# Kernel optimization log

Measured on AMD Instinct MI355X. Metric: run time of the kernel, lower is better.

The kernel has to match this reference:

```python
import jax, jax.numpy as jnp
import numpy as np

LAGS = 2
SLOPE = 0.2  # leaky_relu negative slope


def setup_inputs() -> dict:
    key = jax.random.key(0)
    ks = jax.random.split(key, 12)
    B, T, D, E, H = 32, 1002, 16, 32, 64  # batch, lags+length, latent, embed, hidden
    s = 0.1
    return {
        "x": jax.random.normal(ks[0], (B, T, D), jnp.float32),
        "embeddings": jax.random.normal(ks[1], (B, T, E), jnp.float32),
        # per-latent-dim stacked MLP2 params (num_layers=3 hidden + output head)
        "W0": jax.random.normal(ks[2], (D, H, E + 1), jnp.float32) * s,
        "b0": jax.random.normal(ks[3], (D, H), jnp.float32) * s,
        "W1": jax.random.normal(ks[4], (D, H, H), jnp.float32) * s,
        "b1": jax.random.normal(ks[5], (D, H), jnp.float32) * s,
        "W2": jax.random.normal(ks[6], (D, H, H), jnp.float32) * s,
        "b2": jax.random.normal(ks[7], (D, H), jnp.float32) * s,
        "Wo": jax.random.normal(ks[8], (D, 1, H), jnp.float32) * s,
        "bo": jax.random.normal(ks[9], (D, 1), jnp.float32) * s,
    }


def reference(x, embeddings, W0, b0, W1, b1, W2, b2, Wo, bo):
    B, TL, D = x.shape
    length = TL - LAGS
    E = embeddings.shape[-1]
    N = B * length

    # last element of each unfolded window == x[:, LAGS:, :]
    x_t = x[:, LAGS:, :].reshape(N, D)                       # [N, D]
    emb = embeddings[:, -length:, :].reshape(N, E)           # [N, E]
    # per-dim input: concat(embedding, x_t[:, i]) -> [N, D, E+1]
    inp = jnp.concatenate(
        [jnp.broadcast_to(emb[:, None, :], (N, D, E)), x_t[:, :, None]], axis=-1
    )

    # batched tiny MLPs across latent dims; keep leaky-relu gates for analytic Jacobian
    z0 = jnp.einsum('dhe,nde->ndh', W0, inp) + b0            # [N, D, H]
    g0 = jnp.where(z0 >= 0, 1.0, SLOPE)
    a0 = z0 * g0
    z1 = jnp.einsum('dij,ndj->ndi', W1, a0) + b1
    g1 = jnp.where(z1 >= 0, 1.0, SLOPE)
    a1 = z1 * g1
    z2 = jnp.einsum('dij,ndj->ndi', W2, a1) + b2
    g2 = jnp.where(z2 >= 0, 1.0, SLOPE)
    a2 = z2 * g2
    res = jnp.einsum('doh,ndh->ndo', Wo, a2)[..., 0] + bo[:, 0]   # [N, D]

    # d residual_i / d x_t_i : propagate last input column through the chain
    t = g0 * W0[:, :, -1]                                    # [N, D, H]
    t = g1 * jnp.einsum('dij,ndj->ndi', W1, t)
    t = g2 * jnp.einsum('dij,ndj->ndi', W2, t)
    dJ = jnp.einsum('doh,ndh->ndo', Wo, t)[..., 0]           # [N, D]

    logabsdet = jnp.sum(jnp.log(jnp.abs(dJ)), axis=-1)       # [N]

    residuals = res.reshape(B, length, D)
    log_abs_det_jacobian = logabsdet.reshape(B, length)
    return residuals, log_abs_det_jacobian
```

## Files before the change

kernel.cpp:

```cpp
#include <hip/hip_runtime.h>

constexpr int   kT    = 1002;
constexpr int   kD    = 16;
constexpr int   kE    = 32;
constexpr int   kH    = 64;
constexpr int   kLen  = kT - 2;
constexpr int   kN    = 32 * kLen;
constexpr float kSlope = 0.2f;
constexpr int   AS    = 68;
constexpr int   kWsDwPerD = 15360;

typedef __attribute__((ext_vector_type(8))) short bf16x8;
typedef __attribute__((ext_vector_type(4))) float f32x4;

__device__ __forceinline__ unsigned rne2(float x0, float x1, float &h0, float &h1) {
    unsigned u0 = __float_as_uint(x0), u1 = __float_as_uint(x1);
    unsigned r0 = u0 + 0x7FFFu + ((u0 >> 16) & 1u);
    unsigned r1 = u1 + 0x7FFFu + ((u1 >> 16) & 1u);
    h0 = __uint_as_float(r0 & 0xFFFF0000u);
    h1 = __uint_as_float(r1 & 0xFFFF0000u);
    return __builtin_amdgcn_perm(r1, r0, 0x07060302u);
}

__device__ __forceinline__ void split3_2(float x0, float x1,
                                         unsigned &p1, unsigned &p2, unsigned &p3) {
    float h0, h1; p1 = rne2(x0, x1, h0, h1);
    float e0 = x0 - h0, e1 = x1 - h1;
    float m0, m1; p2 = rne2(e0, e1, m0, m1);
    float f0 = e0 - m0, f1 = e1 - m1;
    float t0, t1; p3 = rne2(f0, f1, t0, t1);
}

__device__ __forceinline__ void split2_2(float x0, float x1, unsigned &p1, unsigned &p2) {
    float h0, h1; p1 = rne2(x0, x1, h0, h1);
    float t0, t1; p2 = rne2(x0 - h0, x1 - h1, t0, t1);
}

union FragU { unsigned u[4]; bf16x8 v; };

__device__ __forceinline__ void splitA3(const float4 a0, const float4 a1,
                                        bf16x8 &A1, bf16x8 &A2, bf16x8 &A3) {
    FragU U1, U2, U3;
    split3_2(a0.x, a0.y, U1.u[0], U2.u[0], U3.u[0]);
    split3_2(a0.z, a0.w, U1.u[1], U2.u[1], U3.u[1]);
    split3_2(a1.x, a1.y, U1.u[2], U2.u[2], U3.u[2]);
    split3_2(a1.z, a1.w, U1.u[3], U2.u[3], U3.u[3]);
    A1 = U1.v; A2 = U2.v; A3 = U3.v;
}

__device__ __forceinline__ void splitA2(const float4 a0, const float4 a1,
                                        bf16x8 &A1, bf16x8 &A2) {
    FragU U1, U2;
    split2_2(a0.x, a0.y, U1.u[0], U2.u[0]);
    split2_2(a0.z, a0.w, U1.u[1], U2.u[1]);
    split2_2(a1.x, a1.y, U1.u[2], U2.u[2]);
    split2_2(a1.z, a1.w, U1.u[3], U2.u[3]);
    A1 = U1.v; A2 = U2.v;
}

__global__ void prep_weights(const float* __restrict__ W0, const float* __restrict__ W1,
                             const float* __restrict__ W2, unsigned* __restrict__ ws,
                             float* __restrict__ out_ld) {
    int id = blockIdx.x * blockDim.x + threadIdx.x;
    if (id < kN) out_ld[id] = 0.f;
    if (id >= 16 * 5120) return;
    int d = id / 5120, rem = id - d * 5120;
    unsigned* wd = ws + (size_t)d * kWsDwPerD;
    float x0, x1; unsigned o1, o2, o3;
    if (rem < 1024) {
        int idx = rem, j2 = idx & 3, ln = (idx >> 2) & 63, nt = (idx >> 8) & 3;
        int n_ = nt * 16 + (ln & 15), k_ = ((ln >> 4) << 3) + 2 * j2;
        const float* g = W0 + (size_t)d * kH * 33;
        x0 = g[n_ * 33 + k_]; x1 = g[n_ * 33 + k_ + 1];
        o1 = idx; o2 = 1024 + idx; o3 = 2048 + idx;
    } else if (rem < 3072) {
        int idx = rem - 1024, j2 = idx & 3, ln = (idx >> 2) & 63;
        int kt = (idx >> 8) & 1, nt = (idx >> 9) & 3;
        int n_ = nt * 16 + (ln & 15), k_ = kt * 32 + ((ln >> 4) << 3) + 2 * j2;
        const float* g = W1 + (size_t)d * kH * kH;
        x0 = g[n_ * 64 + k_]; x1 = g[n_ * 64 + k_ + 1];
        o1 = 3072 + idx; o2 = 5120 + idx; o3 = 7168 + idx;
    } else {
        int idx = rem - 3072, j2 = idx & 3, ln = (idx >> 2) & 63;
        int kt = (idx >> 8) & 1, nt = (idx >> 9) & 3;
        int n_ = nt * 16 + (ln & 15), k_ = kt * 32 + ((ln >> 4) << 3) + 2 * j2;
        const float* g = W2 + (size_t)d * kH * kH;
        x0 = g[n_ * 64 + k_]; x1 = g[n_ * 64 + k_ + 1];
        o1 = 9216 + idx; o2 = 11264 + idx; o3 = 13312 + idx;
    }
    unsigned p1, p2, p3; split3_2(x0, x1, p1, p2, p3);
    wd[o1] = p1; wd[o2] = p2; wd[o3] = p3;
}

#define MFMA(A, B, C) __builtin_amdgcn_mfma_f32_16x16x32_bf16((A), (B), (C), 0, 0, 0)

__device__ __forceinline__ void layer64_f(f32x4 acc[2][4],
                                          const float* r0, const float* r1,
                                          const unsigned* w1, const unsigned* w2,
                                          const unsigned* w3, int lane, int q) {
    #pragma unroll
    for (int kt = 0; kt < 2; ++kt) {
        bf16x8 A1[2], A2[2], A3[2];
        {
            const float4 a0 = *(const float4*)(r0 + kt * 32 + q * 8);
            const float4 a1 = *(const float4*)(r0 + kt * 32 + q * 8 + 4);
            splitA3(a0, a1, A1[0], A2[0], A3[0]);
            const float4 b0_ = *(const float4*)(r1 + kt * 32 + q * 8);
            const float4 b1_ = *(const float4*)(r1 + kt * 32 + q * 8 + 4);
            splitA3(b0_, b1_, A1[1], A2[1], A3[1]);
        }
        bf16x8 B[4];
        #pragma unroll
        for (int nt = 0; nt < 4; ++nt) B[nt] = *(const bf16x8*)(w1 + (((nt * 2 + kt) * 64 + lane) << 2));
        #pragma unroll
        for (int nt = 0; nt < 4; ++nt)
            #pragma unroll
            for (int mt = 0; mt < 2; ++mt) {
                acc[mt][nt] = MFMA(A3[mt], B[nt], acc[mt][nt]);
                acc[mt][nt] = MFMA(A2[mt], B[nt], acc[mt][nt]);
                acc[mt][nt] = MFMA(A1[mt], B[nt], acc[mt][nt]);
            }
        #pragma unroll
        for (int nt = 0; nt < 4; ++nt) B[nt] = *(const bf16x8*)(w2 + (((nt * 2 + kt) * 64 + lane) << 2));
        #pragma unroll
        for (int nt = 0; nt < 4; ++nt)
            #pragma unroll
            for (int mt = 0; mt < 2; ++mt) {
                acc[mt][nt] = MFMA(A2[mt], B[nt], acc[mt][nt]);
                acc[mt][nt] = MFMA(A1[mt], B[nt], acc[mt][nt]);
            }
        #pragma unroll
        for (int nt = 0; nt < 4; ++nt) B[nt] = *(const bf16x8*)(w3 + (((nt * 2 + kt) * 64 + lane) << 2));
        #pragma unroll
        for (int nt = 0; nt < 4; ++nt)
            #pragma unroll
            for (int mt = 0; mt < 2; ++mt)
                acc[mt][nt] = MFMA(A1[mt], B[nt], acc[mt][nt]);
    }
}

__device__ __forceinline__ void layer64_j(f32x4 acc[2][4],
                                          const float* r0, const float* r1,
                                          const unsigned* w1, const unsigned* w2,
                                          int lane, int q) {
    #pragma unroll
    for (int kt = 0; kt < 2; ++kt) {
        bf16x8 A1[2], A2[2];
        {
            const float4 a0 = *(const float4*)(r0 + kt * 32 + q * 8);
            const float4 a1 = *(const float4*)(r0 + kt * 32 + q * 8 + 4);
            splitA2(a0, a1, A1[0], A2[0]);
            const float4 b0_ = *(const float4*)(r1 + kt * 32 + q * 8);
            const float4 b1_ = *(const float4*)(r1 + kt * 32 + q * 8 + 4);
            splitA2(b0_, b1_, A1[1], A2[1]);
        }
        bf16x8 B[4];
        #pragma unroll
        for (int nt = 0; nt < 4; ++nt) B[nt] = *(const bf16x8*)(w1 + (((nt * 2 + kt) * 64 + lane) << 2));
        #pragma unroll
        for (int nt = 0; nt < 4; ++nt)
            #pragma unroll
            for (int mt = 0; mt < 2; ++mt) {
                acc[mt][nt] = MFMA(A2[mt], B[nt], acc[mt][nt]);
                acc[mt][nt] = MFMA(A1[mt], B[nt], acc[mt][nt]);
            }
        #pragma unroll
        for (int nt = 0; nt < 4; ++nt) B[nt] = *(const bf16x8*)(w2 + (((nt * 2 + kt) * 64 + lane) << 2));
        #pragma unroll
        for (int nt = 0; nt < 4; ++nt)
            #pragma unroll
            for (int mt = 0; mt < 2; ++mt)
                acc[mt][nt] = MFMA(A1[mt], B[nt], acc[mt][nt]);
    }
}

__global__ __launch_bounds__(256, 2) void np_mfma_kernel(
    const float* __restrict__ x, const float* __restrict__ emb,
    const float* __restrict__ W0, const float* __restrict__ b0,
    const float* __restrict__ b1, const float* __restrict__ b2,
    const float* __restrict__ Wo, const float* __restrict__ bo,
    const unsigned* __restrict__ ws,
    float* __restrict__ out_res, float* __restrict__ out_ld)
{
    __shared__ __align__(16) float act[128 * AS];

    const int tid  = threadIdx.x;
    const int lane = tid & 63;
    const int wave = __builtin_amdgcn_readfirstlane(tid >> 6);
    const int c = lane & 15, q = lane >> 4;
    const int tb = wave * 32;
    const int d  = blockIdx.y;
    const int nW = blockIdx.x * 128 + tb;

    {
    }
    const int nX  = nW + ((q >> 1) << 4) + c;
    const int bbX = nX / kLen;
    const float xm = x[((size_t)(bbX * kT + (nX - bbX * kLen) + 2)) * kD + d];
    float xr[2][4];
    #pragma unroll
    for (int mt = 0; mt < 2; ++mt)
        #pragma unroll
        for (int r = 0; r < 4; ++r)
            xr[mt][r] = __shfl(xm, mt * 32 + q * 4 + r, 64);

    const float* W0g = W0 + (size_t)d * kH * 33;
    float b0v[4], wov[4], w0xv[4];
    #pragma unroll
    for (int nt = 0; nt < 4; ++nt) {
        const int u = nt * 16 + c;
        b0v[nt]  = b0[d * kH + u];
        wov[nt]  = Wo[d * kH + u];
        w0xv[nt] = W0g[u * 33 + 32];
    }
    const float bov = bo[d];
    const unsigned* wd = ws + (size_t)d * kWsDwPerD;
    const float* r0 = &act[(tb + c) * AS];
    const float* r1 = &act[(tb + 16 + c) * AS];

    unsigned m0 = 0, m1 = 0, m2 = 0;
    f32x4 acc[2][4];

    {
        bf16x8 A1[2], A2[2], A3[2];
        #pragma unroll
        for (int mt = 0; mt < 2; ++mt) {
            const int nA = nW + mt * 16 + c;
            const int bb = nA / kLen;
            const size_t src = (size_t)(bb * kT + (nA - bb * kLen) + 2);
            const float4* ep = (const float4*)(emb + src * kE + q * 8);
            splitA3(ep[0], ep[1], A1[mt], A2[mt], A3[mt]);
        }
        #pragma unroll
        for (int mt = 0; mt < 2; ++mt)
            #pragma unroll
            for (int nt = 0; nt < 4; ++nt) {
                f32x4 a;
                #pragma unroll
                for (int r = 0; r < 4; ++r) a[r] = fmaf(xr[mt][r], w0xv[nt], b0v[nt]);
                acc[mt][nt] = a;
            }
        bf16x8 B[4];
        #pragma unroll
        for (int nt = 0; nt < 4; ++nt) B[nt] = *(const bf16x8*)(wd + ((nt * 64 + lane) << 2));
        #pragma unroll
        for (int nt = 0; nt < 4; ++nt)
            #pragma unroll
            for (int mt = 0; mt < 2; ++mt) {
                acc[mt][nt] = MFMA(A3[mt], B[nt], acc[mt][nt]);
                acc[mt][nt] = MFMA(A2[mt], B[nt], acc[mt][nt]);
                acc[mt][nt] = MFMA(A1[mt], B[nt], acc[mt][nt]);
            }
        #pragma unroll
        for (int nt = 0; nt < 4; ++nt) B[nt] = *(const bf16x8*)(wd + 1024 + ((nt * 64 + lane) << 2));
        #pragma unroll
        for (int nt = 0; nt < 4; ++nt)
            #pragma unroll
            for (int mt = 0; mt < 2; ++mt) {
                acc[mt][nt] = MFMA(A2[mt], B[nt], acc[mt][nt]);
                acc[mt][nt] = MFMA(A1[mt], B[nt], acc[mt][nt]);
            }
        #pragma unroll
        for (int nt = 0; nt < 4; ++nt) B[nt] = *(const bf16x8*)(wd + 2048 + ((nt * 64 + lane) << 2));
        #pragma unroll
        for (int nt = 0; nt < 4; ++nt)
            #pragma unroll
            for (int mt = 0; mt < 2; ++mt)
                acc[mt][nt] = MFMA(A1[mt], B[nt], acc[mt][nt]);
        #pragma unroll
        for (int mt = 0; mt < 2; ++mt)
            #pragma unroll
            for (int nt = 0; nt < 4; ++nt)
                #pragma unroll
                for (int r = 0; r < 4; ++r) {
                    float z = acc[mt][nt][r];
                    bool g = z >= 0.f;
                    m0 |= (unsigned)g << (mt * 16 + nt * 4 + r);
                    act[(tb + mt * 16 + q * 4 + r) * AS + nt * 16 + c] = g ? z : z * kSlope;
                }
    }

    {
        #pragma unroll
        for (int nt = 0; nt < 4; ++nt) {
            const float bv = b1[d * kH + nt * 16 + c];
            #pragma unroll
            for (int mt = 0; mt < 2; ++mt) {
                f32x4 a;
                #pragma unroll
                for (int r = 0; r < 4; ++r) a[r] = bv;
                acc[mt][nt] = a;
            }
        }
        layer64_f(acc, r0, r1, wd + 3072, wd + 5120, wd + 7168, lane, q);
        #pragma unroll
        for (int mt = 0; mt < 2; ++mt)
            #pragma unroll
            for (int nt = 0; nt < 4; ++nt)
                #pragma unroll
                for (int r = 0; r < 4; ++r) {
                    float z = acc[mt][nt][r];
                    bool g = z >= 0.f;
                    m1 |= (unsigned)g << (mt * 16 + nt * 4 + r);
                    act[(tb + mt * 16 + q * 4 + r) * AS + nt * 16 + c] = g ? z : z * kSlope;
                }
    }

    {
        #pragma unroll
        for (int nt = 0; nt < 4; ++nt) {
            const float bv = b2[d * kH + nt * 16 + c];
            #pragma unroll
            for (int mt = 0; mt < 2; ++mt) {
                f32x4 a;
                #pragma unroll
                for (int r = 0; r < 4; ++r) a[r] = bv;
                acc[mt][nt] = a;
            }
        }
        layer64_f(acc, r0, r1, wd + 9216, wd + 11264, wd + 13312, lane, q);
        float pr[2][4] = {{0.f,0.f,0.f,0.f},{0.f,0.f,0.f,0.f}};
        #pragma unroll
        for (int mt = 0; mt < 2; ++mt)
            #pragma unroll
            for (int nt = 0; nt < 4; ++nt)
                #pragma unroll
                for (int r = 0; r < 4; ++r) {
                    float z = acc[mt][nt][r];
                    bool g = z >= 0.f;
                    m2 |= (unsigned)g << (mt * 16 + nt * 4 + r);
                    pr[mt][r] = fmaf(wov[nt], g ? z : z * kSlope, pr[mt][r]);
                }
        #pragma unroll
        for (int mt = 0; mt < 2; ++mt)
            #pragma unroll
            for (int r = 0; r < 4; ++r) {
                #pragma unroll
                for (int s = 1; s < 16; s <<= 1) pr[mt][r] += __shfl_xor(pr[mt][r], s, 16);
            }
        if (c == 0) {
            #pragma unroll
            for (int mt = 0; mt < 2; ++mt)
                #pragma unroll
                for (int r = 0; r < 4; ++r)
                    out_res[(size_t)(nW + mt * 16 + q * 4 + r) * kD + d] = pr[mt][r] + bov;
        }
    }

    #pragma unroll
    for (int mt = 0; mt < 2; ++mt)
        #pragma unroll
        for (int nt = 0; nt < 4; ++nt)
            #pragma unroll
            for (int r = 0; r < 4; ++r)
                act[(tb + mt * 16 + q * 4 + r) * AS + nt * 16 + c] =
                    (((m0 >> (mt * 16 + nt * 4 + r)) & 1u) ? 1.f : kSlope) * w0xv[nt];

    {
        #pragma unroll
        for (int mt = 0; mt < 2; ++mt)
            #pragma unroll
            for (int nt = 0; nt < 4; ++nt) acc[mt][nt] = (f32x4){0.f, 0.f, 0.f, 0.f};
        layer64_j(acc, r0, r1, wd + 3072, wd + 5120, lane, q);
        #pragma unroll
        for (int mt = 0; mt < 2; ++mt)
            #pragma unroll
            for (int nt = 0; nt < 4; ++nt)
                #pragma unroll
                for (int r = 0; r < 4; ++r)
                    act[(tb + mt * 16 + q * 4 + r) * AS + nt * 16 + c] =
                        (((m1 >> (mt * 16 + nt * 4 + r)) & 1u) ? 1.f : kSlope) * acc[mt][nt][r];
    }

    {
        #pragma unroll
        for (int mt = 0; mt < 2; ++mt)
            #pragma unroll
            for (int nt = 0; nt < 4; ++nt) acc[mt][nt] = (f32x4){0.f, 0.f, 0.f, 0.f};
        layer64_j(acc, r0, r1, wd + 9216, wd + 11264, lane, q);
        float pr[2][4] = {{0.f,0.f,0.f,0.f},{0.f,0.f,0.f,0.f}};
        #pragma unroll
        for (int mt = 0; mt < 2; ++mt)
            #pragma unroll
            for (int nt = 0; nt < 4; ++nt)
                #pragma unroll
                for (int r = 0; r < 4; ++r) {
                    float t = (((m2 >> (mt * 16 + nt * 4 + r)) & 1u) ? 1.f : kSlope) * acc[mt][nt][r];
                    pr[mt][r] = fmaf(wov[nt], t, pr[mt][r]);
                }
        #pragma unroll
        for (int mt = 0; mt < 2; ++mt)
            #pragma unroll
            for (int r = 0; r < 4; ++r) {
                #pragma unroll
                for (int s = 1; s < 16; s <<= 1) pr[mt][r] += __shfl_xor(pr[mt][r], s, 16);
            }
        if (c == 0) {
            #pragma unroll
            for (int mt = 0; mt < 2; ++mt)
                #pragma unroll
                for (int r = 0; r < 4; ++r)
                    atomicAdd(&out_ld[nW + mt * 16 + q * 4 + r], __logf(fabsf(pr[mt][r])));
        }
    }
}

extern "C" void kernel_launch(void* const* d_in, const int* in_sizes, int n_in,
                              void* d_out, int out_size, void* d_ws, size_t ws_size,
                              hipStream_t stream) {
    const float* x  = (const float*)d_in[0];
    const float* em = (const float*)d_in[1];
    const float* W0 = (const float*)d_in[2];
    const float* b0 = (const float*)d_in[3];
    const float* W1 = (const float*)d_in[4];
    const float* b1 = (const float*)d_in[5];
    const float* W2 = (const float*)d_in[6];
    const float* b2 = (const float*)d_in[7];
    const float* Wo = (const float*)d_in[8];
    const float* bo = (const float*)d_in[9];

    float* out_res = (float*)d_out;
    float* out_ld  = (float*)d_out + (size_t)kN * kD;
    unsigned* ws   = (unsigned*)d_ws;

    prep_weights<<<dim3(16 * 5120 / 256), dim3(256), 0, stream>>>(W0, W1, W2, ws, out_ld);
    np_mfma_kernel<<<dim3(kN / 128, kD), dim3(256), 0, stream>>>(
        x, em, W0, b0, b1, b2, Wo, bo, ws, out_res, out_ld);
}
```

Baseline: 221.0 us.

## Use fp16 split MFMA for Jacobian layers and halve block size

The Jacobian-chain layers now use a two-term fp16 split via cvt_pkrtz and f16 MFMA, with separate fp16-split weight copies precomputed in the workspace, in place of the bf16 two-term split. Blocks shrink from 256 to 128 threads (64 rows per block) to raise the block count and lower shared memory per block. The leaky-relu select is replaced by fmaxf(z, z*slope). The fp16 path trades bf16's exponent range for more mantissa, which risks overflow or underflow on extreme values, and the prep kernel does more work.

```diff
diff --git a/kernel.cpp b/kernel.cpp
--- a/kernel.cpp
+++ b/kernel.cpp
@@ -8,10 +8,12 @@
 constexpr int   kN    = 32 * kLen;
 constexpr float kSlope = 0.2f;
 constexpr int   AS    = 68;
-constexpr int   kWsDwPerD = 15360;
+constexpr int   kWsDwPerD = 23552;
 
 typedef __attribute__((ext_vector_type(8))) short bf16x8;
 typedef __attribute__((ext_vector_type(4))) float f32x4;
+typedef __attribute__((ext_vector_type(2))) __fp16 fp16x2;
+typedef __attribute__((ext_vector_type(8))) _Float16 f16x8;
 
 __device__ __forceinline__ unsigned rne2(float x0, float x1, float &h0, float &h1) {
     unsigned u0 = __float_as_uint(x0), u1 = __float_as_uint(x1);
@@ -29,11 +31,6 @@
     float m0, m1; p2 = rne2(e0, e1, m0, m1);
     float f0 = e0 - m0, f1 = e1 - m1;
     float t0, t1; p3 = rne2(f0, f1, t0, t1);
-}
-
-__device__ __forceinline__ void split2_2(float x0, float x1, unsigned &p1, unsigned &p2) {
-    float h0, h1; p1 = rne2(x0, x1, h0, h1);
-    float t0, t1; p2 = rne2(x0 - h0, x1 - h1, t0, t1);
 }
 
 union FragU { unsigned u[4]; bf16x8 v; };
@@ -48,13 +45,22 @@
     A1 = U1.v; A2 = U2.v; A3 = U3.v;
 }
 
-__device__ __forceinline__ void splitA2(const float4 a0, const float4 a1,
-                                        bf16x8 &A1, bf16x8 &A2) {
-    FragU U1, U2;
-    split2_2(a0.x, a0.y, U1.u[0], U2.u[0]);
-    split2_2(a0.z, a0.w, U1.u[1], U2.u[1]);
-    split2_2(a1.x, a1.y, U1.u[2], U2.u[2]);
-    split2_2(a1.z, a1.w, U1.u[3], U2.u[3]);
+__device__ __forceinline__ void split2h(float x0, float x1, unsigned &p1, unsigned &p2) {
+    fp16x2 h = __builtin_amdgcn_cvt_pkrtz(x0, x1);
+    __builtin_memcpy(&p1, &h, 4);
+    fp16x2 l = __builtin_amdgcn_cvt_pkrtz(x0 - (float)h[0], x1 - (float)h[1]);
+    __builtin_memcpy(&p2, &l, 4);
+}
+
+union FragH { unsigned u[4]; f16x8 v; };
+
+__device__ __forceinline__ void splitA2h(const float4 a0, const float4 a1,
+                                         f16x8 &A1, f16x8 &A2) {
+    FragH U1, U2;
+    split2h(a0.x, a0.y, U1.u[0], U2.u[0]);
+    split2h(a0.z, a0.w, U1.u[1], U2.u[1]);
+    split2h(a1.x, a1.y, U1.u[2], U2.u[2]);
+    split2h(a1.z, a1.w, U1.u[3], U2.u[3]);
     A1 = U1.v; A2 = U2.v;
 }
 
@@ -63,36 +69,50 @@
                              float* __restrict__ out_ld) {
     int id = blockIdx.x * blockDim.x + threadIdx.x;
     if (id < kN) out_ld[id] = 0.f;
-    if (id >= 16 * 5120) return;
-    int d = id / 5120, rem = id - d * 5120;
+    if (id >= 16 * 9216) return;
+    int d = id / 9216, rem = id - d * 9216;
     unsigned* wd = ws + (size_t)d * kWsDwPerD;
-    float x0, x1; unsigned o1, o2, o3;
-    if (rem < 1024) {
-        int idx = rem, j2 = idx & 3, ln = (idx >> 2) & 63, nt = (idx >> 8) & 3;
-        int n_ = nt * 16 + (ln & 15), k_ = ((ln >> 4) << 3) + 2 * j2;
-        const float* g = W0 + (size_t)d * kH * 33;
-        x0 = g[n_ * 33 + k_]; x1 = g[n_ * 33 + k_ + 1];
-        o1 = idx; o2 = 1024 + idx; o3 = 2048 + idx;
-    } else if (rem < 3072) {
-        int idx = rem - 1024, j2 = idx & 3, ln = (idx >> 2) & 63;
+
+    if (rem < 5120) {
+        float x0, x1; unsigned o1, o2, o3;
+        if (rem < 1024) {
+            int idx = rem, j2 = idx & 3, ln = (idx >> 2) & 63, nt = (idx >> 8) & 3;
+            int n_ = nt * 16 + (ln & 15), k_ = ((ln >> 4) << 3) + 2 * j2;
+            const float* g = W0 + (size_t)d * kH * 33;
+            x0 = g[n_ * 33 + k_]; x1 = g[n_ * 33 + k_ + 1];
+            o1 = idx; o2 = 1024 + idx; o3 = 2048 + idx;
+        } else if (rem < 3072) {
+            int idx = rem - 1024, j2 = idx & 3, ln = (idx >> 2) & 63;
+            int kt = (idx >> 8) & 1, nt = (idx >> 9) & 3;
+            int n_ = nt * 16 + (ln & 15), k_ = kt * 32 + ((ln >> 4) << 3) + 2 * j2;
+            const float* g = W1 + (size_t)d * kH * kH;
+            x0 = g[n_ * 64 + k_]; x1 = g[n_ * 64 + k_ + 1];
+            o1 = 3072 + idx; o2 = 5120 + idx; o3 = 7168 + idx;
+        } else {
+            int idx = rem - 3072, j2 = idx & 3, ln = (idx >> 2) & 63;
+            int kt = (idx >> 8) & 1, nt = (idx >> 9) & 3;
+            int n_ = nt * 16 + (ln & 15), k_ = kt * 32 + ((ln >> 4) << 3) + 2 * j2;
+            const float* g = W2 + (size_t)d * kH * kH;
+            x0 = g[n_ * 64 + k_]; x1 = g[n_ * 64 + k_ + 1];
+            o1 = 9216 + idx; o2 = 11264 + idx; o3 = 13312 + idx;
+        }
+        unsigned p1, p2, p3; split3_2(x0, x1, p1, p2, p3);
+        wd[o1] = p1; wd[o2] = p2; wd[o3] = p3;
+    } else {
+        int idx, base; const float* g;
+        if (rem < 7168) { idx = rem - 5120; base = 15360; g = W1 + (size_t)d * kH * kH; }
+        else            { idx = rem - 7168; base = 19456; g = W2 + (size_t)d * kH * kH; }
+        int j2 = idx & 3, ln = (idx >> 2) & 63;
         int kt = (idx >> 8) & 1, nt = (idx >> 9) & 3;
         int n_ = nt * 16 + (ln & 15), k_ = kt * 32 + ((ln >> 4) << 3) + 2 * j2;
-        const float* g = W1 + (size_t)d * kH * kH;
-        x0 = g[n_ * 64 + k_]; x1 = g[n_ * 64 + k_ + 1];
-        o1 = 3072 + idx; o2 = 5120 + idx; o3 = 7168 + idx;
-    } else {
-        int idx = rem - 3072, j2 = idx & 3, ln = (idx >> 2) & 63;
-        int kt = (idx >> 8) & 1, nt = (idx >> 9) & 3;
-        int n_ = nt * 16 + (ln & 15), k_ = kt * 32 + ((ln >> 4) << 3) + 2 * j2;
-        const float* g = W2 + (size_t)d * kH * kH;
-        x0 = g[n_ * 64 + k_]; x1 = g[n_ * 64 + k_ + 1];
-        o1 = 9216 + idx; o2 = 11264 + idx; o3 = 13312 + idx;
-    }
-    unsigned p1, p2, p3; split3_2(x0, x1, p1, p2, p3);
-    wd[o1] = p1; wd[o2] = p2; wd[o3] = p3;
-}
-
-#define MFMA(A, B, C) __builtin_amdgcn_mfma_f32_16x16x32_bf16((A), (B), (C), 0, 0, 0)
+        float x0 = g[n_ * 64 + k_], x1 = g[n_ * 64 + k_ + 1];
+        unsigned p1, p2; split2h(x0, x1, p1, p2);
+        wd[base + idx] = p1; wd[base + 2048 + idx] = p2;
+    }
+}
+
+#define MFMA(A, B, C)  __builtin_amdgcn_mfma_f32_16x16x32_bf16((A), (B), (C), 0, 0, 0)
+#define MFMAH(A, B, C) __builtin_amdgcn_mfma_f32_16x16x32_f16((A), (B), (C), 0, 0, 0)
 
 __device__ __forceinline__ void layer64_f(f32x4 acc[2][4],
                                           const float* r0, const float* r1,
@@ -139,42 +159,42 @@
     }
 }
 
-__device__ __forceinline__ void layer64_j(f32x4 acc[2][4],
-                                          const float* r0, const float* r1,
-                                          const unsigned* w1, const unsigned* w2,
-                                          int lane, int q) {
+__device__ __forceinline__ void layer64_jh(f32x4 acc[2][4],
+                                           const float* r0, const float* r1,
+                                           const unsigned* wl1, const unsigned* wl2,
+                                           int lane, int q) {
     #pragma unroll
     for (int kt = 0; kt < 2; ++kt) {
-        bf16x8 A1[2], A2[2];
+        f16x8 A1[2], A2[2];
         {
             const float4 a0 = *(const float4*)(r0 + kt * 32 + q * 8);
             const float4 a1 = *(const float4*)(r0 + kt * 32 + q * 8 + 4);
-            splitA2(a0, a1, A1[0], A2[0]);
+            splitA2h(a0, a1, A1[0], A2[0]);
             const float4 b0_ = *(const float4*)(r1 + kt * 32 + q * 8);
             const float4 b1_ = *(const float4*)(r1 + kt * 32 + q * 8 + 4);
-            splitA2(b0_, b1_, A1[1], A2[1]);
-        }
-        bf16x8 B[4];
-        #pragma unroll
-        for (int nt = 0; nt < 4; ++nt) B[nt] = *(const bf16x8*)(w1 + (((nt * 2 + kt) * 64 + lane) << 2));
-        #pragma unroll
-        for (int nt = 0; nt < 4; ++nt)
-            #pragma unroll
-            for (int mt = 0; mt < 2; ++mt) {
-                acc[mt][nt] = MFMA(A2[mt], B[nt], acc[mt][nt]);
-                acc[mt][nt] = MFMA(A1[mt], B[nt], acc[mt][nt]);
-            }
-        #pragma unroll
-        for (int nt = 0; nt < 4; ++nt) B[nt] = *(const bf16x8*)(w2 + (((nt * 2 + kt) * 64 + lane) << 2));
+            splitA2h(b0_, b1_, A1[1], A2[1]);
+        }
+        f16x8 B[4];
+        #pragma unroll
+        for (int nt = 0; nt < 4; ++nt) B[nt] = *(const f16x8*)(wl1 + (((nt * 2 + kt) * 64 + lane) << 2));
+        #pragma unroll
+        for (int nt = 0; nt < 4; ++nt)
+            #pragma unroll
+            for (int mt = 0; mt < 2; ++mt) {
+                acc[mt][nt] = MFMAH(A2[mt], B[nt], acc[mt][nt]);
+                acc[mt][nt] = MFMAH(A1[mt], B[nt], acc[mt][nt]);
+            }
+        #pragma unroll
+        for (int nt = 0; nt < 4; ++nt) B[nt] = *(const f16x8*)(wl2 + (((nt * 2 + kt) * 64 + lane) << 2));
         #pragma unroll
         for (int nt = 0; nt < 4; ++nt)
             #pragma unroll
             for (int mt = 0; mt < 2; ++mt)
-                acc[mt][nt] = MFMA(A1[mt], B[nt], acc[mt][nt]);
-    }
-}
-
-__global__ __launch_bounds__(256, 2) void np_mfma_kernel(
+                acc[mt][nt] = MFMAH(A1[mt], B[nt], acc[mt][nt]);
+    }
+}
+
+__global__ __launch_bounds__(128, 2) void np_mfma_kernel(
     const float* __restrict__ x, const float* __restrict__ emb,
     const float* __restrict__ W0, const float* __restrict__ b0,
     const float* __restrict__ b1, const float* __restrict__ b2,
@@ -182,7 +202,7 @@
     const unsigned* __restrict__ ws,
     float* __restrict__ out_res, float* __restrict__ out_ld)
 {
-    __shared__ __align__(16) float act[128 * AS];
+    __shared__ __align__(16) float act[64 * AS];
 
     const int tid  = threadIdx.x;
     const int lane = tid & 63;
@@ -190,10 +210,8 @@
     const int c = lane & 15, q = lane >> 4;
     const int tb = wave * 32;
     const int d  = blockIdx.y;
-    const int nW = blockIdx.x * 128 + tb;
-
-    {
-    }
+    const int nW = blockIdx.x * 64 + tb;
+
     const int nX  = nW + ((q >> 1) << 4) + c;
     const int bbX = nX / kLen;
     const float xm = x[((size_t)(bbX * kT + (nX - bbX * kLen) + 2)) * kD + d];
@@ -274,9 +292,8 @@
                 #pragma unroll
                 for (int r = 0; r < 4; ++r) {
                     float z = acc[mt][nt][r];
-                    bool g = z >= 0.f;
-                    m0 |= (unsigned)g << (mt * 16 + nt * 4 + r);
-                    act[(tb + mt * 16 + q * 4 + r) * AS + nt * 16 + c] = g ? z : z * kSlope;
+                    m0 |= (unsigned)(z >= 0.f) << (mt * 16 + nt * 4 + r);
+                    act[(tb + mt * 16 + q * 4 + r) * AS + nt * 16 + c] = fmaxf(z, z * kSlope);
                 }
     }
 
@@ -300,9 +317,8 @@
                 #pragma unroll
                 for (int r = 0; r < 4; ++r) {
                     float z = acc[mt][nt][r];
-                    bool g = z >= 0.f;
-                    m1 |= (unsigned)g << (mt * 16 + nt * 4 + r);
-                    act[(tb + mt * 16 + q * 4 + r) * AS + nt * 16 + c] = g ? z : z * kSlope;
+                    m1 |= (unsigned)(z >= 0.f) << (mt * 16 + nt * 4 + r);
+                    act[(tb + mt * 16 + q * 4 + r) * AS + nt * 16 + c] = fmaxf(z, z * kSlope);
                 }
     }
 
@@ -327,9 +343,8 @@
                 #pragma unroll
                 for (int r = 0; r < 4; ++r) {
                     float z = acc[mt][nt][r];
-                    bool g = z >= 0.f;
-                    m2 |= (unsigned)g << (mt * 16 + nt * 4 + r);
-                    pr[mt][r] = fmaf(wov[nt], g ? z : z * kSlope, pr[mt][r]);
+                    m2 |= (unsigned)(z >= 0.f) << (mt * 16 + nt * 4 + r);
+                    pr[mt][r] = fmaf(wov[nt], fmaxf(z, z * kSlope), pr[mt][r]);
                 }
         #pragma unroll
         for (int mt = 0; mt < 2; ++mt)
@@ -361,7 +376,7 @@
         for (int mt = 0; mt < 2; ++mt)
             #pragma unroll
             for (int nt = 0; nt < 4; ++nt) acc[mt][nt] = (f32x4){0.f, 0.f, 0.f, 0.f};
-        layer64_j(acc, r0, r1, wd + 3072, wd + 5120, lane, q);
+        layer64_jh(acc, r0, r1, wd + 15360, wd + 17408, lane, q);
         #pragma unroll
         for (int mt = 0; mt < 2; ++mt)
             #pragma unroll
@@ -377,7 +392,7 @@
         for (int mt = 0; mt < 2; ++mt)
             #pragma unroll
             for (int nt = 0; nt < 4; ++nt) acc[mt][nt] = (f32x4){0.f, 0.f, 0.f, 0.f};
-        layer64_j(acc, r0, r1, wd + 9216, wd + 11264, lane, q);
+        layer64_jh(acc, r0, r1, wd + 19456, wd + 21504, lane, q);
         float pr[2][4] = {{0.f,0.f,0.f,0.f},{0.f,0.f,0.f,0.f}};
         #pragma unroll
         for (int mt = 0; mt < 2; ++mt)
@@ -423,7 +438,7 @@
     float* out_ld  = (float*)d_out + (size_t)kN * kD;
     unsigned* ws   = (unsigned*)d_ws;
 
-    prep_weights<<<dim3(16 * 5120 / 256), dim3(256), 0, stream>>>(W0, W1, W2, ws, out_ld);
-    np_mfma_kernel<<<dim3(kN / 128, kD), dim3(256), 0, stream>>>(
+    prep_weights<<<dim3(16 * 9216 / 256), dim3(256), 0, stream>>>(W0, W1, W2, ws, out_ld);
+    np_mfma_kernel<<<dim3(kN / 64, kD), dim3(128), 0, stream>>>(
         x, em, W0, b0, b1, b2, Wo, bo, ws, out_res, out_ld);
 }
```

Result: faster. 184.8 us (-16.4%).
